# Kernel tuning notes

Hardware: AMD Instinct MI355X
Metric: run time of the kernel (lower is better)

## Reference

```python
import jax, jax.numpy as jnp
import numpy as np

N_NODES = 50000
N_EDGES = 800000
IN_FEATS = 256
OUT_FEATS = 64


def setup_inputs() -> dict:
    key = jax.random.key(0)
    k1, k2, k3, k4 = jax.random.split(key, 4)
    feat = jax.random.normal(k1, (N_NODES, IN_FEATS), dtype=jnp.float32)
    # xavier_uniform-like init for weight
    limit = float(np.sqrt(6.0 / (IN_FEATS + OUT_FEATS)))
    weight = jax.random.uniform(k2, (IN_FEATS, OUT_FEATS), dtype=jnp.float32,
                                minval=-limit, maxval=limit)
    bias = jnp.zeros((OUT_FEATS,), dtype=jnp.float32)
    src = jax.random.randint(k3, (N_EDGES,), 0, N_NODES, dtype=jnp.int32)
    dst = jax.random.randint(k4, (N_EDGES,), 0, N_NODES, dtype=jnp.int32)
    return {"feat": feat, "weight": weight, "bias": bias, "src": src, "dst": dst}


def reference(feat, weight, bias, src, dst):
    # GCN GraphConv with norm='both', edge_weight=None, activation=None.
    n = feat.shape[0]
    ones_e = jnp.ones(src.shape[0], dtype=feat.dtype)
    out_deg = jnp.clip(jax.ops.segment_sum(ones_e, src, num_segments=n), 1.0)
    in_deg = jnp.clip(jax.ops.segment_sum(ones_e, dst, num_segments=n), 1.0)

    # left/both pre-normalization by out-degree^{-1/2}
    feat_src = feat * (out_deg ** -0.5)[:, None]

    # lin_before_mp: in_feats (256) > out_feats (64) -> project first
    h = feat_src @ weight  # [N, out_feats]

    # copy_u + sum aggregation: gather from src, scatter-add to dst
    rst = jax.ops.segment_sum(h[src], dst, num_segments=n)  # [N, out_feats]

    # right/both post-normalization by in-degree^{-1/2}, then bias
    rst = rst * (in_deg ** -0.5)[:, None] + bias
    return rst
```

## Files before the change

### kernel.cpp

```cpp
#include <hip/hip_runtime.h>
#include <hip/hip_bf16.h>

#define N_NODES 50000
#define N_EDGES 800000
#define IN_F 256
#define OUT_F 64
#define NBUCKET 196
#define HCOPIES 32
#define EDGES_PER_COPY 25000
#define HWORDS 25000
#define PBLOCKS 200
#define EDGES_PER_PBLOCK 4000
#define MAXB 6144

using bf16x8 = __attribute__((ext_vector_type(8))) short;
using f32x4  = __attribute__((ext_vector_type(4))) float;

__global__ __launch_bounds__(1024)
void hist_kernel(const int* __restrict__ src, const int* __restrict__ dst,
                 unsigned* __restrict__ scratch) {
    __shared__ unsigned lh[HWORDS];
    int tid = threadIdx.x, b = blockIdx.x;
    const int* idx = (b < HCOPIES) ? src : dst;
    int k = b & 31;
    int e0 = k * EDGES_PER_COPY;
    for (int i = tid; i < HWORDS; i += 1024) lh[i] = 0;
    __syncthreads();
    for (int i = tid; i < EDGES_PER_COPY; i += 1024) {
        int id = idx[e0 + i];
        atomicAdd(&lh[id >> 1], (id & 1) ? 0x10000u : 1u);
    }
    __syncthreads();
    unsigned* outp = scratch + (size_t)b * HWORDS;
    for (int i = tid; i < HWORDS; i += 1024) outp[i] = lh[i];
}

__global__ void reduce_kernel(const unsigned* __restrict__ scratch,
                              int* __restrict__ cnt_out, int* __restrict__ cnt_in) {
    int t = blockIdx.x * blockDim.x + threadIdx.x;
    if (t >= 2 * HWORDS) return;
    int side = (t >= HWORDS);
    int j = side ? t - HWORDS : t;
    const unsigned* base = scratch + (size_t)(side ? HCOPIES : 0) * HWORDS + j;
    unsigned lo = 0, hi = 0;
    for (int k = 0; k < HCOPIES; ++k) {
        unsigned v = base[(size_t)k * HWORDS];
        lo += v & 0xFFFFu; hi += v >> 16;
    }
    int* dstp = side ? cnt_in : cnt_out;
    dstp[2 * j] = (int)lo;
    dstp[2 * j + 1] = (int)hi;
}

__global__ void scan_kernel(const int* __restrict__ cnt_in,
                            int* __restrict__ bucket_off, int* __restrict__ bucket_cursor) {
    __shared__ int tot[256];
    int t = threadIdx.x;
    int s = 0;
    if (t < NBUCKET) {
        int base = t * 256;
        int lim = min(256, N_NODES - base);
        for (int i = 0; i < lim; ++i) s += cnt_in[base + i];
    }
    tot[t] = s;
    __syncthreads();
    for (int off = 1; off < 256; off <<= 1) {
        int v = (t >= off) ? tot[t - off] : 0;
        __syncthreads();
        tot[t] += v;
        __syncthreads();
    }
    if (t < NBUCKET) {
        int excl = tot[t] - s;
        bucket_off[t] = excl;
        bucket_cursor[t * 16] = excl;
    }
    if (t == NBUCKET - 1) bucket_off[NBUCKET] = tot[t];
}

__global__ __launch_bounds__(1024)
void partition_kernel(const int* __restrict__ src, const int* __restrict__ dst,
                      int* __restrict__ bucket_cursor, unsigned* __restrict__ recs) {
    __shared__ int lcnt[NBUCKET], lbase[NBUCKET];
    int tid = threadIdx.x;
    int e0 = blockIdx.x * EDGES_PER_PBLOCK;
    if (tid < NBUCKET) lcnt[tid] = 0;
    __syncthreads();
    unsigned rec[4]; int bkt[4], rnk[4];
#pragma unroll
    for (int j = 0; j < 4; ++j) {
        int i = j * 1024 + tid;
        bkt[j] = -1;
        if (i < EDGES_PER_PBLOCK) {
            int e = e0 + i;
            int s = src[e], d = dst[e];
            bkt[j] = d >> 8;
            rec[j] = (unsigned)s | ((unsigned)(d & 255) << 16);
            rnk[j] = atomicAdd(&lcnt[bkt[j]], 1);
        }
    }
    __syncthreads();
    if (tid < NBUCKET) lbase[tid] = atomicAdd(&bucket_cursor[tid * 16], lcnt[tid]);
    __syncthreads();
#pragma unroll
    for (int j = 0; j < 4; ++j)
        if (bkt[j] >= 0) recs[lbase[bkt[j]] + rnk[j]] = rec[j];
}

__global__ __launch_bounds__(256)
void gemm_kernel(const float* __restrict__ feat, const float* __restrict__ weight,
                 const int* __restrict__ cnt_out, __hip_bfloat16* __restrict__ h) {
    __shared__ __align__(16) short Wt[64 * 256];
    int tid = threadIdx.x;

#pragma unroll
    for (int it = 0; it < 16; ++it) {
        int idx = it * 256 + tid;
        int k  = idx >> 4;
        int n4 = (idx & 15) * 4;
        float4 wv = *(const float4*)&weight[k * OUT_F + n4];
#pragma unroll
        for (int j = 0; j < 4; ++j) {
            int n = n4 + j;
            __hip_bfloat16 bv = __float2bfloat16((&wv.x)[j]);
            int byte = (n * 512 + k * 2) ^ ((n & 7) << 4);
            *(short*)((char*)Wt + byte) = *(short*)&bv;
        }
    }

    int lane = tid & 63, w = tid >> 6;
    int rowbase = blockIdx.x * 64 + w * 16;
    int arow = rowbase + (lane & 15);
    int arc = min(arow, N_NODES - 1);
    float sc = rsqrtf((float)max(cnt_out[arc], 1));
    const float* ap = &feat[arc * IN_F + (lane >> 4) * 8];
    __syncthreads();

    f32x4 acc[4];
#pragma unroll
    for (int c = 0; c < 4; ++c) acc[c] = (f32x4){0.f, 0.f, 0.f, 0.f};

#pragma unroll
    for (int ks = 0; ks < 8; ++ks) {
        float4 a0 = *(const float4*)(ap + ks * 32);
        float4 a1 = *(const float4*)(ap + ks * 32 + 4);
        bf16x8 af;
#pragma unroll
        for (int j = 0; j < 4; ++j) {
            __hip_bfloat16 b0 = __float2bfloat16((&a0.x)[j] * sc);
            __hip_bfloat16 b1 = __float2bfloat16((&a1.x)[j] * sc);
            af[j]     = *(short*)&b0;
            af[j + 4] = *(short*)&b1;
        }
        int kb = ks * 64 + (lane >> 4) * 16;
#pragma unroll
        for (int c = 0; c < 4; ++c) {
            int n = c * 16 + (lane & 15);
            int byte = (n * 512 + kb) ^ ((n & 7) << 4);
            bf16x8 bfv = *(const bf16x8*)((const char*)Wt + byte);
            acc[c] = __builtin_amdgcn_mfma_f32_16x16x32_bf16(af, bfv, acc[c], 0, 0, 0);
        }
    }

#pragma unroll
    for (int c = 0; c < 4; ++c) {
#pragma unroll
        for (int r = 0; r < 4; ++r) {
            int row = rowbase + (lane >> 4) * 4 + r;
            if (row < N_NODES)
                h[row * OUT_F + c * 16 + (lane & 15)] = __float2bfloat16(acc[c][r]);
        }
    }
}

__global__ __launch_bounds__(1024)
void aggregate_kernel(const __hip_bfloat16* __restrict__ h, const unsigned* __restrict__ recs,
                      const int* __restrict__ bucket_off,
                      const float* __restrict__ bias, float* __restrict__ out) {
    __shared__ int cnt[256], off[256], cur[256];
    __shared__ unsigned short order[MAXB];
    int tid = threadIdx.x, lane = tid & 63, w = tid >> 6;
    int b = blockIdx.x;
    if (tid < 256) { cnt[tid] = 0; cur[tid] = 0; }
    __syncthreads();
    int start = bucket_off[b], end = bucket_off[b + 1];
    int n = end - start;

    for (int i = tid; i < n; i += 1024)
        atomicAdd(&cnt[(recs[start + i] >> 16) & 255u], 1);
    __syncthreads();

    if (tid < 256) off[tid] = cnt[tid];
    __syncthreads();
    for (int o = 1; o < 256; o <<= 1) {
        int y = (tid < 256 && tid >= o) ? off[tid - o] : 0;
        __syncthreads();
        if (tid < 256) off[tid] += y;
        __syncthreads();
    }

    for (int i = tid; i < n; i += 1024) {
        unsigned rec = recs[start + i];
        int dl = (rec >> 16) & 255u;
        int r = atomicAdd(&cur[dl], 1);
        int pos = off[dl] - cnt[dl] + r;
        if (pos < MAXB) order[pos] = (unsigned short)(rec & 0xFFFFu);
    }
    __syncthreads();

    float bv = bias[lane];
    int gbase = b * 256;
    for (int nd = w; nd < 256; nd += 16) {
        int g = gbase + nd;
        if (g >= N_NODES) continue;
        int m = cnt[nd];
        int s0 = off[nd] - m;
        float acc = 0.f;
        int k = 0;
        for (; k + 4 <= m; k += 4) {
            int a0 = order[s0 + k], a1 = order[s0 + k + 1];
            int a2 = order[s0 + k + 2], a3 = order[s0 + k + 3];
            acc += __bfloat162float(h[a0 * OUT_F + lane]) + __bfloat162float(h[a1 * OUT_F + lane])
                 + __bfloat162float(h[a2 * OUT_F + lane]) + __bfloat162float(h[a3 * OUT_F + lane]);
        }
        for (; k < m; ++k) acc += __bfloat162float(h[order[s0 + k] * OUT_F + lane]);
        float sc = rsqrtf((float)max(m, 1));
        out[g * OUT_F + lane] = fmaf(acc, sc, bv);
    }
}

extern "C" void kernel_launch(void* const* d_in, const int* in_sizes, int n_in,
                              void* d_out, int out_size, void* d_ws, size_t ws_size,
                              hipStream_t stream) {
    const float* feat   = (const float*)d_in[0];
    const float* weight = (const float*)d_in[1];
    const float* bias   = (const float*)d_in[2];
    const int*   src    = (const int*)d_in[3];
    const int*   dst    = (const int*)d_in[4];
    float* out = (float*)d_out;

    int* ws            = (int*)d_ws;
    int* cnt_out       = ws;
    int* cnt_in        = ws + 50000;
    int* bucket_off    = ws + 100000;
    int* bucket_cursor = ws + 100224;
    unsigned* scratch  = (unsigned*)(ws + 103424);
    unsigned* recs     = (unsigned*)(ws + 1703424);
    __hip_bfloat16* h  = (__hip_bfloat16*)(ws + 2503424);

    hist_kernel<<<2 * HCOPIES, 1024, 0, stream>>>(src, dst, scratch);
    reduce_kernel<<<(2 * HWORDS + 1023) / 1024, 1024, 0, stream>>>(scratch, cnt_out, cnt_in);
    scan_kernel<<<1, 256, 0, stream>>>(cnt_in, bucket_off, bucket_cursor);
    partition_kernel<<<PBLOCKS, 1024, 0, stream>>>(src, dst, bucket_cursor, recs);
    gemm_kernel<<<(N_NODES + 63) / 64, 256, 0, stream>>>(feat, weight, cnt_out, h);
    aggregate_kernel<<<NBUCKET, 1024, 0, stream>>>(h, recs, bucket_off, bias, out);
}
```

Before: 179.5 us.

## Replace in-degree histogram and scan with fixed-capacity per-bucket edge slots

Drops the destination histogram, its reduction and the bucket prefix-scan kernel. Edges are partitioned into fixed-capacity slots per destination bucket using zeroed atomic cursors, and the aggregate kernel reads each bucket's count from its cursor. This removes a kernel launch and half of the histogram work, at the cost of silently dropping edges if a bucket exceeds its capacity and of an added memset.

Result: faster. 163.5 us (-8.9%).

```diff
diff --git a/kernel.cpp b/kernel.cpp
--- a/kernel.cpp
+++ b/kernel.cpp
@@ -6,28 +6,25 @@
 #define IN_F 256
 #define OUT_F 64
 #define NBUCKET 196
+#define CAPB 6144
 #define HCOPIES 32
 #define EDGES_PER_COPY 25000
 #define HWORDS 25000
 #define PBLOCKS 200
 #define EDGES_PER_PBLOCK 4000
-#define MAXB 6144
 
 using bf16x8 = __attribute__((ext_vector_type(8))) short;
 using f32x4  = __attribute__((ext_vector_type(4))) float;
 
 __global__ __launch_bounds__(1024)
-void hist_kernel(const int* __restrict__ src, const int* __restrict__ dst,
-                 unsigned* __restrict__ scratch) {
+void hist_kernel(const int* __restrict__ src, unsigned* __restrict__ scratch) {
     __shared__ unsigned lh[HWORDS];
     int tid = threadIdx.x, b = blockIdx.x;
-    const int* idx = (b < HCOPIES) ? src : dst;
-    int k = b & 31;
-    int e0 = k * EDGES_PER_COPY;
+    int e0 = b * EDGES_PER_COPY;
     for (int i = tid; i < HWORDS; i += 1024) lh[i] = 0;
     __syncthreads();
     for (int i = tid; i < EDGES_PER_COPY; i += 1024) {
-        int id = idx[e0 + i];
+        int id = src[e0 + i];
         atomicAdd(&lh[id >> 1], (id & 1) ? 0x10000u : 1u);
     }
     __syncthreads();
@@ -36,46 +33,16 @@
 }
 
 __global__ void reduce_kernel(const unsigned* __restrict__ scratch,
-                              int* __restrict__ cnt_out, int* __restrict__ cnt_in) {
-    int t = blockIdx.x * blockDim.x + threadIdx.x;
-    if (t >= 2 * HWORDS) return;
-    int side = (t >= HWORDS);
-    int j = side ? t - HWORDS : t;
-    const unsigned* base = scratch + (size_t)(side ? HCOPIES : 0) * HWORDS + j;
+                              int* __restrict__ cnt_out) {
+    int j = blockIdx.x * blockDim.x + threadIdx.x;
+    if (j >= HWORDS) return;
     unsigned lo = 0, hi = 0;
     for (int k = 0; k < HCOPIES; ++k) {
-        unsigned v = base[(size_t)k * HWORDS];
+        unsigned v = scratch[(size_t)k * HWORDS + j];
         lo += v & 0xFFFFu; hi += v >> 16;
     }
-    int* dstp = side ? cnt_in : cnt_out;
-    dstp[2 * j] = (int)lo;
-    dstp[2 * j + 1] = (int)hi;
-}
-
-__global__ void scan_kernel(const int* __restrict__ cnt_in,
-                            int* __restrict__ bucket_off, int* __restrict__ bucket_cursor) {
-    __shared__ int tot[256];
-    int t = threadIdx.x;
-    int s = 0;
-    if (t < NBUCKET) {
-        int base = t * 256;
-        int lim = min(256, N_NODES - base);
-        for (int i = 0; i < lim; ++i) s += cnt_in[base + i];
-    }
-    tot[t] = s;
-    __syncthreads();
-    for (int off = 1; off < 256; off <<= 1) {
-        int v = (t >= off) ? tot[t - off] : 0;
-        __syncthreads();
-        tot[t] += v;
-        __syncthreads();
-    }
-    if (t < NBUCKET) {
-        int excl = tot[t] - s;
-        bucket_off[t] = excl;
-        bucket_cursor[t * 16] = excl;
-    }
-    if (t == NBUCKET - 1) bucket_off[NBUCKET] = tot[t];
+    cnt_out[2 * j] = (int)lo;
+    cnt_out[2 * j + 1] = (int)hi;
 }
 
 __global__ __launch_bounds__(1024)
@@ -103,8 +70,13 @@
     if (tid < NBUCKET) lbase[tid] = atomicAdd(&bucket_cursor[tid * 16], lcnt[tid]);
     __syncthreads();
 #pragma unroll
-    for (int j = 0; j < 4; ++j)
-        if (bkt[j] >= 0) recs[lbase[bkt[j]] + rnk[j]] = rec[j];
+    for (int j = 0; j < 4; ++j) {
+        if (bkt[j] >= 0) {
+            int pos = lbase[bkt[j]] + rnk[j];
+            if (pos < CAPB)
+                recs[(size_t)bkt[j] * CAPB + pos] = rec[j];
+        }
+    }
 }
 
 __global__ __launch_bounds__(256)
@@ -175,16 +147,16 @@
 
 __global__ __launch_bounds__(1024)
 void aggregate_kernel(const __hip_bfloat16* __restrict__ h, const unsigned* __restrict__ recs,
-                      const int* __restrict__ bucket_off,
+                      const int* __restrict__ bucket_cursor,
                       const float* __restrict__ bias, float* __restrict__ out) {
     __shared__ int cnt[256], off[256], cur[256];
-    __shared__ unsigned short order[MAXB];
+    __shared__ unsigned short order[CAPB];
     int tid = threadIdx.x, lane = tid & 63, w = tid >> 6;
     int b = blockIdx.x;
     if (tid < 256) { cnt[tid] = 0; cur[tid] = 0; }
     __syncthreads();
-    int start = bucket_off[b], end = bucket_off[b + 1];
-    int n = end - start;
+    size_t start = (size_t)b * CAPB;
+    int n = min(bucket_cursor[b * 16], CAPB);
 
     for (int i = tid; i < n; i += 1024)
         atomicAdd(&cnt[(recs[start + i] >> 16) & 255u], 1);
@@ -204,7 +176,7 @@
         int dl = (rec >> 16) & 255u;
         int r = atomicAdd(&cur[dl], 1);
         int pos = off[dl] - cnt[dl] + r;
-        if (pos < MAXB) order[pos] = (unsigned short)(rec & 0xFFFFu);
+        order[pos] = (unsigned short)(rec & 0xFFFFu);
     }
     __syncthreads();
 
@@ -241,17 +213,16 @@
 
     int* ws            = (int*)d_ws;
     int* cnt_out       = ws;
-    int* cnt_in        = ws + 50000;
-    int* bucket_off    = ws + 100000;
-    int* bucket_cursor = ws + 100224;
-    unsigned* scratch  = (unsigned*)(ws + 103424);
-    unsigned* recs     = (unsigned*)(ws + 1703424);
-    __hip_bfloat16* h  = (__hip_bfloat16*)(ws + 2503424);
-
-    hist_kernel<<<2 * HCOPIES, 1024, 0, stream>>>(src, dst, scratch);
-    reduce_kernel<<<(2 * HWORDS + 1023) / 1024, 1024, 0, stream>>>(scratch, cnt_out, cnt_in);
-    scan_kernel<<<1, 256, 0, stream>>>(cnt_in, bucket_off, bucket_cursor);
+    int* bucket_cursor = ws + 50048;
+    unsigned* scratch  = (unsigned*)(ws + 53248);
+    unsigned* recs     = (unsigned*)(ws + 853248);
+    __hip_bfloat16* h  = (__hip_bfloat16*)(ws + 2057472);
+
+    hipMemsetAsync(bucket_cursor, 0, 3136 * sizeof(int), stream);
+
+    hist_kernel<<<HCOPIES, 1024, 0, stream>>>(src, scratch);
+    reduce_kernel<<<(HWORDS + 1023) / 1024, 1024, 0, stream>>>(scratch, cnt_out);
     partition_kernel<<<PBLOCKS, 1024, 0, stream>>>(src, dst, bucket_cursor, recs);
     gemm_kernel<<<(N_NODES + 63) / 64, 256, 0, stream>>>(feat, weight, cnt_out, h);
-    aggregate_kernel<<<NBUCKET, 1024, 0, stream>>>(h, recs, bucket_off, bias, out);
-}
+    aggregate_kernel<<<NBUCKET, 1024, 0, stream>>>(h, recs, bucket_cursor, bias, out);
+}
```
